# Kernel optimization log

Measured on AMD Instinct MI355X. Metric: run time of the kernel, lower is better.

Reference implementation:

```python
import jax, jax.numpy as jnp
import numpy as np
import math

E = 256          # embed_dim
H = 16           # num_heads
D = E // H       # qkv_dim = 16; also ms_hidden_dim per head
B, R, C = 4, 512, 512


def setup_inputs() -> dict:
    key = jax.random.key(0)
    ks = jax.random.split(key, 9)
    x1 = jax.random.normal(ks[0], (B, R, E), dtype=jnp.float32)
    x2 = jax.random.normal(ks[1], (B, C, E), dtype=jnp.float32)
    cost_mat = jax.random.uniform(ks[2], (B, R, C), dtype=jnp.float32)
    attn_mask = jnp.ones((B, R, C), dtype=bool)
    s = 0.02
    Wqv1 = jax.random.normal(ks[3], (2 * E, E), dtype=jnp.float32) * s   # nn.Linear(E, 2E)
    W1ms = jax.random.normal(ks[4], (H * D, 2 * H), dtype=jnp.float32) * s  # lin1: 2H -> H*D
    W2ms = jax.random.normal(ks[5], (H, H * D), dtype=jnp.float32) * s      # lin2: H*D -> H
    Wo1 = jax.random.normal(ks[6], (E, E), dtype=jnp.float32) * s
    Wo2 = jax.random.normal(ks[7], (E, E), dtype=jnp.float32) * s
    return {"x1": x1, "x2": x2, "cost_mat": cost_mat, "attn_mask": attn_mask,
            "Wqv1": Wqv1, "W1ms": W1ms, "W2ms": W2ms, "Wo1": Wo1, "Wo2": Wo2}


def _apply_weights_and_combine(dots, v):
    # dots: [b h r c], v: [b h c d]
    logits = dots / jnp.std(dots, ddof=1)           # torch .std() is unbiased
    weights = jax.nn.softmax(logits, axis=-1)
    weights = jnp.where(jnp.isnan(weights), 0.0, weights)  # nan_to_num(0)
    out = jnp.einsum('bhrc,bhcd->bhrd', weights, v)
    b, h, s, d = out.shape
    return out.transpose(0, 2, 1, 3).reshape(b, s, h * d)  # 'b h s d -> b s (h d)'


def reference(x1, x2, cost_mat, attn_mask, Wqv1, W1ms, W2ms, Wo1, Wo2):
    b, r, e = x1.shape
    c = x2.shape[1]
    norm = 1.0 / math.sqrt(D)
    # NOTE: source applies Wqv1 to BOTH x1 and x2 (Wkv2 is unused) - kept faithful.
    qv1 = (x1 @ Wqv1.T).reshape(b, r, 2, H, D)
    q = qv1[:, :, 0].transpose(0, 2, 1, 3)   # b h r d
    v1 = qv1[:, :, 1].transpose(0, 2, 1, 3)
    kv2 = (x2 @ Wqv1.T).reshape(b, c, 2, H, D)
    k = kv2[:, :, 0].transpose(0, 2, 1, 3)   # b h c d
    v2 = kv2[:, :, 1].transpose(0, 2, 1, 3)

    dot = norm * jnp.einsum('bhrd,bhcd->bhrc', q, k)       # b h r c
    cost = jnp.broadcast_to(cost_mat[:, None], dot.shape)   # b h r c
    # MixedScoreFF: stack -> 'b h r c s -> b r c (h s)' -> lin1 -> relu -> lin2
    two = jnp.stack([dot, cost], axis=-1)                    # b h r c 2
    two = two.transpose(0, 2, 3, 1, 4).reshape(b, r, c, 2 * H)
    ms1 = jax.nn.relu(two @ W1ms.T)                          # b r c (H*D)
    ms2 = ms1 @ W2ms.T                                       # b r c H
    dot = ms2.transpose(0, 3, 1, 2)                          # b h r c

    mask = jnp.broadcast_to(attn_mask[:, None], dot.shape)
    dot = jnp.where(mask, dot, -jnp.inf)

    h1 = _apply_weights_and_combine(dot, v2) @ Wo1.T                      # b r e
    h2 = _apply_weights_and_combine(dot.transpose(0, 1, 3, 2), v1) @ Wo2.T  # b c e
    return h1, h2
```

## Files before the change

### kernel.cpp

```cpp
#include <hip/hip_runtime.h>
#include <hip/hip_bf16.h>
#include <math.h>
#include <float.h>

#define BB 4
#define RR 512
#define CC 512
#define EE 256
#define HH 16
#define DD 16

typedef short bf16x8 __attribute__((ext_vector_type(8)));
typedef float f32x4 __attribute__((ext_vector_type(4)));
typedef unsigned int uint4v __attribute__((ext_vector_type(4)));
typedef unsigned short u16;
typedef unsigned int u32;

__device__ __forceinline__ void split_bf16(float v, u16& hi, u16& lo)
{
    u32 u = __builtin_bit_cast(u32, v);
    hi = (u16)(u >> 16);
    float hf = __builtin_bit_cast(float, u & 0xffff0000u);
    lo = (u16)(__builtin_bit_cast(u32, v - hf) >> 16);
}

__device__ __forceinline__ void split2(float v0, float v1, u32& hi, u32& lo)
{
    u32 u0 = __builtin_bit_cast(u32, v0);
    u32 u1 = __builtin_bit_cast(u32, v1);
    hi = (u0 >> 16) | (u1 & 0xffff0000u);
    float l0 = v0 - __builtin_bit_cast(float, u0 & 0xffff0000u);
    float l1 = v1 - __builtin_bit_cast(float, u1 & 0xffff0000u);
    lo = (__builtin_bit_cast(u32, l0) >> 16) |
         (__builtin_bit_cast(u32, l1) & 0xffff0000u);
}

__device__ __forceinline__ void split2_cvt(float v0, float v1, u32& hi, u32& lo)
{
    u32 h;
    asm("v_cvt_pk_bf16_f32 %0, %1, %2" : "=v"(h) : "v"(v0), "v"(v1));
    float h0 = __builtin_bit_cast(float, h << 16);
    float h1 = __builtin_bit_cast(float, h & 0xffff0000u);
    float r0 = v0 - h0, r1 = v1 - h1;
    u32 lo_;
    asm("v_cvt_pk_bf16_f32 %0, %1, %2" : "=v"(lo_) : "v"(r0), "v"(r1));
    hi = h; lo = lo_;
}

__device__ __forceinline__ bf16x8 mk8(u32 a, u32 b, u32 c, u32 d)
{
    return __builtin_bit_cast(bf16x8, (uint4v){a, b, c, d});
}

__global__ __launch_bounds__(256) void split_multi(
    const float* __restrict__ s0, u16* __restrict__ h0, u16* __restrict__ l0, int n0,
    const float* __restrict__ s1, u16* __restrict__ h1, u16* __restrict__ l1, int n1,
    const float* __restrict__ s2, u16* __restrict__ h2, u16* __restrict__ l2, int n2,
    const float* __restrict__ s3, u16* __restrict__ h3, u16* __restrict__ l3, int n3,
    const float* __restrict__ s4, u16* __restrict__ h4, u16* __restrict__ l4, int n4)
{
    const float* src; u16* dh; u16* dl; int n;
    switch (blockIdx.y) {
        case 0: src = s0; dh = h0; dl = l0; n = n0; break;
        case 1: src = s1; dh = h1; dl = l1; n = n1; break;
        case 2: src = s2; dh = h2; dl = l2; n = n2; break;
        case 3: src = s3; dh = h3; dl = l3; n = n3; break;
        default: src = s4; dh = h4; dl = l4; n = n4; break;
    }
    for (int i = blockIdx.x * 256 + threadIdx.x; i < n; i += gridDim.x * 256) {
        float4 v = reinterpret_cast<const float4*>(src)[i];
        u32 a0, b0, a1, b1;
        split2(v.x, v.y, a0, b0);
        split2(v.z, v.w, a1, b1);
        reinterpret_cast<uint2*>(dh)[i] = make_uint2(a0, a1);
        reinterpret_cast<uint2*>(dl)[i] = make_uint2(b0, b1);
    }
}

__global__ __launch_bounds__(256) void gemm_mfma(
    const u16* __restrict__ Xh0, const u16* __restrict__ Xl0,
    const u16* __restrict__ Wh0, const u16* __restrict__ Wl0,
    float* __restrict__ Y0,
    const u16* __restrict__ Xh1, const u16* __restrict__ Xl1,
    const u16* __restrict__ Wh1, const u16* __restrict__ Wl1,
    float* __restrict__ Y1,
    int M, int N)
{
    const int t = threadIdx.x;
    const int w = t >> 6, l = t & 63, g = l >> 4, q = l & 15;
    const int z = blockIdx.z;
    const u16* __restrict__ Xh = z ? Xh1 : Xh0;
    const u16* __restrict__ Xl = z ? Xl1 : Xl0;
    const u16* __restrict__ Wh = z ? Wh1 : Wh0;
    const u16* __restrict__ Wl = z ? Wl1 : Wl0;
    float* __restrict__ Y = z ? Y1 : Y0;

    const int m0 = blockIdx.x * 64, n0 = blockIdx.y * 64;
    const size_t arow = (size_t)(m0 + w * 16 + q) * 256;

    f32x4 acc[4] = {};
    #pragma unroll 2
    for (int k0 = 0; k0 < 256; k0 += 32) {
        const bf16x8 ah = *reinterpret_cast<const bf16x8*>(Xh + arow + k0 + g * 8);
        const bf16x8 al = *reinterpret_cast<const bf16x8*>(Xl + arow + k0 + g * 8);
        #pragma unroll
        for (int nt = 0; nt < 4; ++nt) {
            const size_t brow = (size_t)(n0 + nt * 16 + q) * 256;
            const bf16x8 bh = *reinterpret_cast<const bf16x8*>(Wh + brow + k0 + g * 8);
            const bf16x8 bl = *reinterpret_cast<const bf16x8*>(Wl + brow + k0 + g * 8);
            acc[nt] = __builtin_amdgcn_mfma_f32_16x16x32_bf16(ah, bl, acc[nt], 0, 0, 0);
            acc[nt] = __builtin_amdgcn_mfma_f32_16x16x32_bf16(al, bh, acc[nt], 0, 0, 0);
            acc[nt] = __builtin_amdgcn_mfma_f32_16x16x32_bf16(ah, bh, acc[nt], 0, 0, 0);
        }
    }
    #pragma unroll
    for (int nt = 0; nt < 4; ++nt)
        #pragma unroll
        for (int rg = 0; rg < 4; ++rg)
            Y[(size_t)(m0 + w * 16 + g * 4 + rg) * N + n0 + nt * 16 + q] = acc[nt][rg];
}

__global__ void pack_weights(const float* __restrict__ W1,
                             const float* __restrict__ W2,
                             u16* __restrict__ Wb1h, u16* __restrict__ Wb1l,
                             u16* __restrict__ Wb2h, u16* __restrict__ Wb2l)
{
    const int t = threadIdx.x;
    for (int idx = t; idx < 16 * 64 * 8; idx += 256) {
        int nt = idx >> 9, rem = idx & 511, l = rem >> 3, i = rem & 7;
        int k = ((l >> 4) << 3) + i, j = nt * 16 + (l & 15);
        float v = 0.f;
        if (k < 16) {
            v = 0.25f * W1[j * 32 + 2 * k];
        } else if (k == 16) {
            float s = 0.f;
            #pragma unroll
            for (int h = 0; h < 16; ++h) s += W1[j * 32 + 2 * h + 1];
            v = s;
        }
        u16 hi, lo; split_bf16(v, hi, lo);
        Wb1h[idx] = hi; Wb1l[idx] = lo;
    }
    for (int idx = t; idx < 8 * 64 * 8; idx += 256) {
        int kt = idx >> 9, rem = idx & 511, l = rem >> 3, i = rem & 7;
        int jj = kt * 32 + ((l >> 4) << 3) + i, h = l & 15;
        float v = W2[h * 256 + jj];
        u16 hi, lo; split_bf16(v, hi, lo);
        Wb2h[idx] = hi; Wb2l[idx] = lo;
    }
}

__global__ __launch_bounds__(256, 4) void score_ff(
    const float* __restrict__ qv1, const float* __restrict__ kv2,
    const float* __restrict__ cost,
    const u16* __restrict__ Wb1h, const u16* __restrict__ Wb1l,
    const u16* __restrict__ Wb2h, const u16* __restrict__ Wb2l,
    float* __restrict__ S, float* __restrict__ stats)
{
    __shared__ __align__(16) u16 Fhi[16][16][16];
    __shared__ __align__(16) u16 Flo[16][16][16];
    __shared__ __align__(16) float Hs[4][16][32];
    __shared__ float costS[16][16];
    __shared__ __align__(16) f32x4 red[2][4][64];

    const int t = threadIdx.x;
    const int w = t >> 6, l = t & 63;
    const int g = l >> 4, q = l & 15;
    const int b = blockIdx.z;
    const int r0 = blockIdx.y * 16, c0 = blockIdx.x * 16;

    {
        int rr = t >> 4, cc = t & 15;
        costS[rr][cc] = cost[((size_t)b * RR + r0 + rr) * CC + c0 + cc];
    }

    #pragma unroll
    for (int hh = 0; hh < 4; ++hh) {
        const int h = w * 4 + hh;
        bf16x8 qhi = {}, qlo = {}, khi = {}, klo = {};
        if (g < 2) {
            const float4* qp = reinterpret_cast<const float4*>(
                qv1 + ((size_t)b * RR + r0 + q) * (2 * EE) + h * 16 + g * 8);
            const float4* kp = reinterpret_cast<const float4*>(
                kv2 + ((size_t)b * CC + c0 + q) * (2 * EE) + h * 16 + g * 8);
            float4 q0 = qp[0], q1 = qp[1];
            float4 k0 = kp[0], k1 = kp[1];
            u32 a0, a1, a2, a3, b0, b1, b2, b3;
            split2(q0.x, q0.y, a0, b0); split2(q0.z, q0.w, a1, b1);
            split2(q1.x, q1.y, a2, b2); split2(q1.z, q1.w, a3, b3);
            qhi = mk8(a0, a1, a2, a3); qlo = mk8(b0, b1, b2, b3);
            split2(k0.x, k0.y, a0, b0); split2(k0.z, k0.w, a1, b1);
            split2(k1.x, k1.y, a2, b2); split2(k1.z, k1.w, a3, b3);
            khi = mk8(a0, a1, a2, a3); klo = mk8(b0, b1, b2, b3);
        }
        f32x4 d = {0.f, 0.f, 0.f, 0.f};
        d = __builtin_amdgcn_mfma_f32_16x16x32_bf16(qhi, klo, d, 0, 0, 0);
        d = __builtin_amdgcn_mfma_f32_16x16x32_bf16(qlo, khi, d, 0, 0, 0);
        d = __builtin_amdgcn_mfma_f32_16x16x32_bf16(qhi, khi, d, 0, 0, 0);
        #pragma unroll
        for (int rg = 0; rg < 4; ++rg) {
            int r = g * 4 + rg;
            u16 hi, lo; split_bf16(d[rg], hi, lo);
            u32 ad = ((u32)(r * 512 + q * 32 + h * 2)) ^
                     (((((u32)r & 7u) ^ ((u32)q >> 2)) & 7u) << 4);
            *(u16*)((char*)Fhi + ad) = hi;
            *(u16*)((char*)Flo + ad) = lo;
        }
    }

    bf16x8 w1h_r[4], w1l_r[4], w2h_r[2], w2l_r[2];
    #pragma unroll
    for (int jt = 0; jt < 4; ++jt) {
        int nt = w * 4 + jt;
        w1h_r[jt] = *reinterpret_cast<const bf16x8*>(Wb1h + ((nt * 64 + l) << 3));
        w1l_r[jt] = *reinterpret_cast<const bf16x8*>(Wb1l + ((nt * 64 + l) << 3));
    }
    #pragma unroll
    for (int kk = 0; kk < 2; ++kk) {
        int kt = w * 2 + kk;
        w2h_r[kk] = *reinterpret_cast<const bf16x8*>(Wb2h + ((kt * 64 + l) << 3));
        w2l_r[kk] = *reinterpret_cast<const bf16x8*>(Wb2l + ((kt * 64 + l) << 3));
    }
    __syncthreads();

    float lsum = 0.f, lsq = 0.f;
    char* hw = (char*)&Hs[w][0][0];
    const u32 hswz = ((u32)q & 7u) << 4;

    for (int rr = 0; rr < 16; ++rr) {
        bf16x8 fhi = {}, flo = {};
        {
            const u32 fswz = (((((u32)rr & 7u) ^ ((u32)q >> 2)) & 7u) << 4);
            if (g < 2) {
                u32 fa = ((u32)(rr * 512 + q * 32 + g * 16)) ^ fswz;
                fhi = *reinterpret_cast<const bf16x8*>((char*)Fhi + fa);
                flo = *reinterpret_cast<const bf16x8*>((char*)Flo + fa);
            } else if (g == 2) {
                u16 chi, clo; split_bf16(costS[rr][q], chi, clo);
                fhi[0] = (short)chi; flo[0] = (short)clo;
            }
        }

        f32x4 acc2 = {0.f, 0.f, 0.f, 0.f};
        #pragma unroll
        for (int ch = 0; ch < 2; ++ch) {
            #pragma unroll
            for (int jt2 = 0; jt2 < 2; ++jt2) {
                int jt = ch * 2 + jt2;
                f32x4 a = {0.f, 0.f, 0.f, 0.f};
                a = __builtin_amdgcn_mfma_f32_16x16x32_bf16(w1h_r[jt], flo, a, 0, 0, 0);
                a = __builtin_amdgcn_mfma_f32_16x16x32_bf16(w1l_r[jt], fhi, a, 0, 0, 0);
                a = __builtin_amdgcn_mfma_f32_16x16x32_bf16(w1h_r[jt], fhi, a, 0, 0, 0);
                f32x4 hrel;
                #pragma unroll
                for (int rg = 0; rg < 4; ++rg) hrel[rg] = fmaxf(a[rg], 0.f);
                u32 ad = ((u32)(q * 128 + jt2 * 64 + g * 16)) ^ hswz;
                *reinterpret_cast<f32x4*>(hw + ad) = hrel;
            }
            const f32x4 h0 = *reinterpret_cast<const f32x4*>(
                hw + (((u32)(q * 128 + g * 32)) ^ hswz));
            const f32x4 h1 = *reinterpret_cast<const f32x4*>(
                hw + (((u32)(q * 128 + g * 32 + 16)) ^ hswz));
            u32 hh0, hl0, hh1, hl1, hh2, hl2, hh3, hl3;
            split2_cvt(h0[0], h0[1], hh0, hl0); split2_cvt(h0[2], h0[3], hh1, hl1);
            split2_cvt(h1[0], h1[1], hh2, hl2); split2_cvt(h1[2], h1[3], hh3, hl3);
            const bf16x8 ha = mk8(hh0, hh1, hh2, hh3);
            const bf16x8 hb = mk8(hl0, hl1, hl2, hl3);
            acc2 = __builtin_amdgcn_mfma_f32_16x16x32_bf16(ha, w2l_r[ch], acc2, 0, 0, 0);
            acc2 = __builtin_amdgcn_mfma_f32_16x16x32_bf16(hb, w2h_r[ch], acc2, 0, 0, 0);
            acc2 = __builtin_amdgcn_mfma_f32_16x16x32_bf16(ha, w2h_r[ch], acc2, 0, 0, 0);
        }

        if (rr > 0) {
            int pr = rr - 1, par = pr & 1;
            f32x4 s4 = red[par][0][l] + red[par][1][l] + red[par][2][l] + red[par][3][l];
            float v = (w & 2) ? ((w & 1) ? s4[3] : s4[2])
                              : ((w & 1) ? s4[1] : s4[0]);
            lsum += v; lsq = fmaf(v, v, lsq);
            S[(((size_t)b * HH + q) * RR + r0 + pr) * CC + c0 + g * 4 + w] = v;
        }

        red[rr & 1][w][l] = acc2;
        __syncthreads();
    }
    {
        f32x4 s4 = red[1][0][l] + red[1][1][l] + red[1][2][l] + red[1][3][l];
        float v = (w & 2) ? ((w & 1) ? s4[3] : s4[2])
                          : ((w & 1) ? s4[1] : s4[0]);
        lsum += v; lsq = fmaf(v, v, lsq);
        S[(((size_t)b * HH + q) * RR + r0 + 15) * CC + c0 + g * 4 + w] = v;
    }

    #pragma unroll
    for (int s = 32; s; s >>= 1) {
        lsum += __shfl_xor(lsum, s);
        lsq  += __shfl_xor(lsq, s);
    }
    if (l == 0) {
        int bucket = (((blockIdx.x + blockIdx.y * 8 + blockIdx.z * 32) << 2) + w) & 127;
        atomicAdd(&stats[2 * bucket],     lsum);
        atomicAdd(&stats[2 * bucket + 1], lsq);
    }
}

__global__ void finalize_std(const float* __restrict__ stats,
                             float* __restrict__ invstd)
{
    double sum = 0.0, sq = 0.0;
    for (int i = 0; i < 128; ++i) { sum += (double)stats[2 * i]; sq += (double)stats[2 * i + 1]; }
    double N = (double)BB * HH * RR * CC;
    double mean = sum / N;
    double var = (sq - N * mean * mean) / (N - 1.0);
    float inv = (var > 0.0 && isfinite(var)) ? (float)(1.0 / sqrt(var)) : nanf("");
    *invstd = inv;
}

__global__ __launch_bounds__(256, 4) void attn_rows(
    const float* __restrict__ S, const float* __restrict__ kv2,
    const float* __restrict__ invstd_p,
    u16* __restrict__ a1h, u16* __restrict__ a1l)
{
    __shared__ __align__(16) u16 Vthi[16 * 512];
    __shared__ __align__(16) u16 Vtlo[16 * 512];

    const int t = threadIdx.x;
    const int w = t >> 6, l = t & 63;
    const int g = l >> 4, q = l & 15;
    const int b = blockIdx.z, h = blockIdx.y;
    const int r0 = blockIdx.x * 64 + w * 16;
    const float inv = *invstd_p;

    {
        const float* v0p = kv2 + ((size_t)b * CC + 2 * t) * (2 * EE) + EE + h * DD;
        const float* v1p = v0p + 2 * EE;
        float4 va[4], vb[4];
        #pragma unroll
        for (int j = 0; j < 4; ++j) {
            va[j] = reinterpret_cast<const float4*>(v0p)[j];
            vb[j] = reinterpret_cast<const float4*>(v1p)[j];
        }
        const float* vaf = reinterpret_cast<const float*>(va);
        const float* vbf = reinterpret_cast<const float*>(vb);
        #pragma unroll
        for (int d = 0; d < 16; ++d) {
            u32 hi, lo; split2(vaf[d], vbf[d], hi, lo);
            u32 ad = ((u32)d * 1024 + (u32)t * 4) ^ (((u32)d & 7) << 4);
            *reinterpret_cast<u32*>((char*)Vthi + ad) = hi;
            *reinterpret_cast<u32*>((char*)Vtlo + ad) = lo;
        }
    }
    __syncthreads();

    float lsum = 0.f;
    f32x4 acc = {0.f, 0.f, 0.f, 0.f};
    #pragma unroll 4
    for (int kt = 0; kt < 16; ++kt) {
        const float* sp = S + (((size_t)b * HH + h) * RR + r0 + q) * CC + kt * 32 + g * 8;
        float4 s0 = reinterpret_cast<const float4*>(sp)[0];
        float4 s1 = reinterpret_cast<const float4*>(sp)[1];
        float p[8];
        p[0] = __expf(s0.x * inv); p[1] = __expf(s0.y * inv);
        p[2] = __expf(s0.z * inv); p[3] = __expf(s0.w * inv);
        p[4] = __expf(s1.x * inv); p[5] = __expf(s1.y * inv);
        p[6] = __expf(s1.z * inv); p[7] = __expf(s1.w * inv);
        lsum += (p[0] + p[1]) + (p[2] + p[3]) + (p[4] + p[5]) + (p[6] + p[7]);
        u32 ph[4], pl[4];
        split2(p[0], p[1], ph[0], pl[0]); split2(p[2], p[3], ph[1], pl[1]);
        split2(p[4], p[5], ph[2], pl[2]); split2(p[6], p[7], ph[3], pl[3]);
        const bf16x8 phi = mk8(ph[0], ph[1], ph[2], ph[3]);
        const bf16x8 plo = mk8(pl[0], pl[1], pl[2], pl[3]);
        u32 A = ((u32)q * 1024 + (u32)(kt * 64 + g * 16)) ^ (((u32)q & 7) << 4);
        const bf16x8 vhi = *reinterpret_cast<const bf16x8*>((char*)Vthi + A);
        const bf16x8 vlo = *reinterpret_cast<const bf16x8*>((char*)Vtlo + A);
        acc = __builtin_amdgcn_mfma_f32_16x16x32_bf16(phi, vlo, acc, 0, 0, 0);
        acc = __builtin_amdgcn_mfma_f32_16x16x32_bf16(plo, vhi, acc, 0, 0, 0);
        acc = __builtin_amdgcn_mfma_f32_16x16x32_bf16(phi, vhi, acc, 0, 0, 0);
    }
    lsum += __shfl_xor(lsum, 16);
    lsum += __shfl_xor(lsum, 32);

    #pragma unroll
    for (int rg = 0; rg < 4; ++rg) {
        int row = g * 4 + rg;
        float L = __shfl(lsum, row);
        bool valid = (L > 0.f) && isfinite(L);
        float rl = valid ? 1.f / L : 0.f;
        float v = acc[rg] * rl;
        u16 hi, lo; split_bf16(v, hi, lo);
        size_t off = ((size_t)b * RR + r0 + row) * EE + h * DD + q;
        a1h[off] = hi; a1l[off] = lo;
    }
}

__global__ __launch_bounds__(256, 4) void attn_cols(
    const float* __restrict__ S, const float* __restrict__ qv1,
    const float* __restrict__ invstd_p,
    u16* __restrict__ a2h, u16* __restrict__ a2l)
{
    __shared__ __align__(16) u16 Vthi[16 * 512];
    __shared__ __align__(16) u16 Vtlo[16 * 512];

    const int t = threadIdx.x;
    const int w = t >> 6, l = t & 63;
    const int g = l >> 4, q = l & 15;
    const int b = blockIdx.z, h = blockIdx.y;
    const int c0 = blockIdx.x * 64 + w * 16;
    const float inv = *invstd_p;

    {
        const float* v0p = qv1 + ((size_t)b * RR + 2 * t) * (2 * EE) + EE + h * DD;
        const float* v1p = v0p + 2 * EE;
        float4 va[4], vb[4];
        #pragma unroll
        for (int j = 0; j < 4; ++j) {
            va[j] = reinterpret_cast<const float4*>(v0p)[j];
            vb[j] = reinterpret_cast<const float4*>(v1p)[j];
        }
        const float* vaf = reinterpret_cast<const float*>(va);
        const float* vbf = reinterpret_cast<const float*>(vb);
        #pragma unroll
        for (int d = 0; d < 16; ++d) {
            u32 hi, lo; split2(vaf[d], vbf[d], hi, lo);
            u32 ad = ((u32)d * 1024 + (u32)t * 4) ^ (((u32)d & 7) << 4);
            *reinterpret_cast<u32*>((char*)Vthi + ad) = hi;
            *reinterpret_cast<u32*>((char*)Vtlo + ad) = lo;
        }
    }
    __syncthreads();

    float lsum = 0.f;
    f32x4 acc = {0.f, 0.f, 0.f, 0.f};
    #pragma unroll 4
    for (int kt = 0; kt < 16; ++kt) {
        const float* sp = S + (((size_t)b * HH + h) * RR + kt * 32 + g * 8) * CC + c0 + q;
        float p[8];
        #pragma unroll
        for (int i = 0; i < 8; ++i)
            p[i] = __expf(sp[(size_t)i * CC] * inv);
        lsum += (p[0] + p[1]) + (p[2] + p[3]) + (p[4] + p[5]) + (p[6] + p[7]);
        u32 ph[4], pl[4];
        split2(p[0], p[1], ph[0], pl[0]); split2(p[2], p[3], ph[1], pl[1]);
        split2(p[4], p[5], ph[2], pl[2]); split2(p[6], p[7], ph[3], pl[3]);
        const bf16x8 phi = mk8(ph[0], ph[1], ph[2], ph[3]);
        const bf16x8 plo = mk8(pl[0], pl[1], pl[2], pl[3]);
        u32 A = ((u32)q * 1024 + (u32)(kt * 64 + g * 16)) ^ (((u32)q & 7) << 4);
        const bf16x8 vhi = *reinterpret_cast<const bf16x8*>((char*)Vthi + A);
        const bf16x8 vlo = *reinterpret_cast<const bf16x8*>((char*)Vtlo + A);
        acc = __builtin_amdgcn_mfma_f32_16x16x32_bf16(phi, vlo, acc, 0, 0, 0);
        acc = __builtin_amdgcn_mfma_f32_16x16x32_bf16(plo, vhi, acc, 0, 0, 0);
        acc = __builtin_amdgcn_mfma_f32_16x16x32_bf16(phi, vhi, acc, 0, 0, 0);
    }
    lsum += __shfl_xor(lsum, 16);
    lsum += __shfl_xor(lsum, 32);

    #pragma unroll
    for (int rg = 0; rg < 4; ++rg) {
        int row = g * 4 + rg;
        float L = __shfl(lsum, row);
        bool valid = (L > 0.f) && isfinite(L);
        float rl = valid ? 1.f / L : 0.f;
        float v = acc[rg] * rl;
        u16 hi, lo; split_bf16(v, hi, lo);
        size_t off = ((size_t)b * CC + c0 + row) * EE + h * DD + q;
        a2h[off] = hi; a2l[off] = lo;
    }
}

extern "C" void kernel_launch(void* const* d_in, const int* in_sizes, int n_in,
                              void* d_out, int out_size, void* d_ws, size_t ws_size,
                              hipStream_t stream)
{
    const float* x1   = (const float*)d_in[0];
    const float* x2   = (const float*)d_in[1];
    const float* cost = (const float*)d_in[2];
    const float* Wqv1 = (const float*)d_in[4];
    const float* W1ms = (const float*)d_in[5];
    const float* W2ms = (const float*)d_in[6];
    const float* Wo1  = (const float*)d_in[7];
    const float* Wo2  = (const float*)d_in[8];

    float* ws    = (float*)d_ws;
    float* qv1   = ws;
    float* kv2   = qv1 + (size_t)1048576;
    float* S     = kv2 + (size_t)1048576;
    float* A1    = S + (size_t)16777216;
    float* A2    = A1 + (size_t)524288;
    float* stats = A2 + (size_t)524288;
    float* invstd = stats + 256;
    u16* Wb1h = (u16*)(invstd + 4);
    u16* Wb1l = Wb1h + 8192;
    u16* Wb2h = Wb1l + 8192;
    u16* Wb2l = Wb2h + 4096;
    u16* x1h  = Wb2l + 4096;
    u16* x1l  = x1h + 524288;
    u16* x2h  = x1l + 524288;
    u16* x2l  = x2h + 524288;
    u16* wqh  = x2l + 524288;
    u16* wql  = wqh + 131072;
    u16* wo1h = wql + 131072;
    u16* wo1l = wo1h + 65536;
    u16* wo2h = wo1l + 65536;
    u16* wo2l = wo2h + 65536;
    u16* a1h  = wo2l + 65536;
    u16* a1l  = a1h + 524288;
    u16* a2h  = a1l + 524288;
    u16* a2l  = a2h + 524288;

    hipMemsetAsync(stats, 0, 256 * sizeof(float), stream);

    pack_weights<<<1, 256, 0, stream>>>(W1ms, W2ms, Wb1h, Wb1l, Wb2h, Wb2l);
    split_multi<<<dim3(128, 5), 256, 0, stream>>>(
        x1, x1h, x1l, 131072,
        x2, x2h, x2l, 131072,
        Wqv1, wqh, wql, 32768,
        Wo1, wo1h, wo1l, 16384,
        Wo2, wo2h, wo2l, 16384);

    gemm_mfma<<<dim3(32, 8, 2), 256, 0, stream>>>(
        x1h, x1l, wqh, wql, qv1,
        x2h, x2l, wqh, wql, kv2, 2048, 512);

    score_ff<<<dim3(32, 32, 4), 256, 0, stream>>>(qv1, kv2, cost,
                                                  Wb1h, Wb1l, Wb2h, Wb2l, S, stats);
    finalize_std<<<1, 1, 0, stream>>>(stats, invstd);
    attn_rows<<<dim3(8, 16, 4), 256, 0, stream>>>(S, kv2, invstd, a1h, a1l);
    attn_cols<<<dim3(8, 16, 4), 256, 0, stream>>>(S, qv1, invstd, a2h, a2l);

    gemm_mfma<<<dim3(32, 4, 2), 256, 0, stream>>>(
        a1h, a1l, wo1h, wo1l, (float*)d_out,
        a2h, a2l, wo2h, wo2l, (float*)d_out + (size_t)2048 * 256, 2048, 256);
}
```

Baseline: 198.1 us.

## Fuse attention row/col kernels, inline std finalize, merge weight packing launch

Merges attn_rows and attn_cols into one launch with a doubled grid. The single-thread finalize_std kernel is replaced by a per-wave shuffle reduction of the stats in every attention block. pack_weights becomes an extra blockIdx.y slice of split_multi. score_ff drops its double-buffered reduction in favour of a single buffer with two barriers per row, and its occupancy hint rises to 5 blocks. The aim is fewer launches and less serialization, at the cost of extra syncs in score_ff and of computing the variance in float instead of double.

```diff
diff --git a/kernel.cpp b/kernel.cpp
--- a/kernel.cpp
+++ b/kernel.cpp
@@ -52,13 +52,60 @@
     return __builtin_bit_cast(bf16x8, (uint4v){a, b, c, d});
 }
 
+__device__ __forceinline__ float compute_invstd(const float* __restrict__ stats,
+                                                int l)
+{
+    float se = stats[2 * l] + stats[2 * l + 128];
+    float sq = stats[2 * l + 1] + stats[2 * l + 129];
+    #pragma unroll
+    for (int s = 32; s; s >>= 1) {
+        se += __shfl_xor(se, s);
+        sq += __shfl_xor(sq, s);
+    }
+    const float Nf = 16777216.f;
+    float mean = se / Nf;
+    float var = (sq - Nf * mean * mean) / (Nf - 1.f);
+    bool ok = (var > 0.f) && isfinite(var);
+    return ok ? (1.f / sqrtf(var)) : __builtin_nanf("");
+}
+
 __global__ __launch_bounds__(256) void split_multi(
     const float* __restrict__ s0, u16* __restrict__ h0, u16* __restrict__ l0, int n0,
     const float* __restrict__ s1, u16* __restrict__ h1, u16* __restrict__ l1, int n1,
     const float* __restrict__ s2, u16* __restrict__ h2, u16* __restrict__ l2, int n2,
     const float* __restrict__ s3, u16* __restrict__ h3, u16* __restrict__ l3, int n3,
-    const float* __restrict__ s4, u16* __restrict__ h4, u16* __restrict__ l4, int n4)
-{
+    const float* __restrict__ s4, u16* __restrict__ h4, u16* __restrict__ l4, int n4,
+    const float* __restrict__ W1, const float* __restrict__ W2,
+    u16* __restrict__ Wb1h, u16* __restrict__ Wb1l,
+    u16* __restrict__ Wb2h, u16* __restrict__ Wb2l)
+{
+    const int t = threadIdx.x;
+    if (blockIdx.y == 5) {
+        if (blockIdx.x != 0) return;
+        for (int idx = t; idx < 16 * 64 * 8; idx += 256) {
+            int nt = idx >> 9, rem = idx & 511, l = rem >> 3, i = rem & 7;
+            int k = ((l >> 4) << 3) + i, j = nt * 16 + (l & 15);
+            float v = 0.f;
+            if (k < 16) {
+                v = 0.25f * W1[j * 32 + 2 * k];
+            } else if (k == 16) {
+                float s = 0.f;
+                #pragma unroll
+                for (int h = 0; h < 16; ++h) s += W1[j * 32 + 2 * h + 1];
+                v = s;
+            }
+            u16 hi, lo; split_bf16(v, hi, lo);
+            Wb1h[idx] = hi; Wb1l[idx] = lo;
+        }
+        for (int idx = t; idx < 8 * 64 * 8; idx += 256) {
+            int kt = idx >> 9, rem = idx & 511, l = rem >> 3, i = rem & 7;
+            int jj = kt * 32 + ((l >> 4) << 3) + i, h = l & 15;
+            float v = W2[h * 256 + jj];
+            u16 hi, lo; split_bf16(v, hi, lo);
+            Wb2h[idx] = hi; Wb2l[idx] = lo;
+        }
+        return;
+    }
     const float* src; u16* dh; u16* dl; int n;
     switch (blockIdx.y) {
         case 0: src = s0; dh = h0; dl = l0; n = n0; break;
@@ -67,7 +114,7 @@
         case 3: src = s3; dh = h3; dl = l3; n = n3; break;
         default: src = s4; dh = h4; dl = l4; n = n4; break;
     }
-    for (int i = blockIdx.x * 256 + threadIdx.x; i < n; i += gridDim.x * 256) {
+    for (int i = blockIdx.x * 256 + t; i < n; i += gridDim.x * 256) {
         float4 v = reinterpret_cast<const float4*>(src)[i];
         u32 a0, b0, a1, b1;
         split2(v.x, v.y, a0, b0);
@@ -120,37 +167,7 @@
             Y[(size_t)(m0 + w * 16 + g * 4 + rg) * N + n0 + nt * 16 + q] = acc[nt][rg];
 }
 
-__global__ void pack_weights(const float* __restrict__ W1,
-                             const float* __restrict__ W2,
-                             u16* __restrict__ Wb1h, u16* __restrict__ Wb1l,
-                             u16* __restrict__ Wb2h, u16* __restrict__ Wb2l)
-{
-    const int t = threadIdx.x;
-    for (int idx = t; idx < 16 * 64 * 8; idx += 256) {
-        int nt = idx >> 9, rem = idx & 511, l = rem >> 3, i = rem & 7;
-        int k = ((l >> 4) << 3) + i, j = nt * 16 + (l & 15);
-        float v = 0.f;
-        if (k < 16) {
-            v = 0.25f * W1[j * 32 + 2 * k];
-        } else if (k == 16) {
-            float s = 0.f;
-            #pragma unroll
-            for (int h = 0; h < 16; ++h) s += W1[j * 32 + 2 * h + 1];
-            v = s;
-        }
-        u16 hi, lo; split_bf16(v, hi, lo);
-        Wb1h[idx] = hi; Wb1l[idx] = lo;
-    }
-    for (int idx = t; idx < 8 * 64 * 8; idx += 256) {
-        int kt = idx >> 9, rem = idx & 511, l = rem >> 3, i = rem & 7;
-        int jj = kt * 32 + ((l >> 4) << 3) + i, h = l & 15;
-        float v = W2[h * 256 + jj];
-        u16 hi, lo; split_bf16(v, hi, lo);
-        Wb2h[idx] = hi; Wb2l[idx] = lo;
-    }
-}
-
-__global__ __launch_bounds__(256, 4) void score_ff(
+__global__ __launch_bounds__(256, 5) void score_ff(
     const float* __restrict__ qv1, const float* __restrict__ kv2,
     const float* __restrict__ cost,
     const u16* __restrict__ Wb1h, const u16* __restrict__ Wb1l,
@@ -161,7 +178,7 @@
     __shared__ __align__(16) u16 Flo[16][16][16];
     __shared__ __align__(16) float Hs[4][16][32];
     __shared__ float costS[16][16];
-    __shared__ __align__(16) f32x4 red[2][4][64];
+    __shared__ __align__(16) f32x4 red[4][64];
 
     const int t = threadIdx.x;
     const int w = t >> 6, l = t & 63;
@@ -271,24 +288,16 @@
             acc2 = __builtin_amdgcn_mfma_f32_16x16x32_bf16(ha, w2h_r[ch], acc2, 0, 0, 0);
         }
 
-        if (rr > 0) {
-            int pr = rr - 1, par = pr & 1;
-            f32x4 s4 = red[par][0][l] + red[par][1][l] + red[par][2][l] + red[par][3][l];
+        red[w][l] = acc2;
+        __syncthreads();
+        {
+            f32x4 s4 = red[0][l] + red[1][l] + red[2][l] + red[3][l];
             float v = (w & 2) ? ((w & 1) ? s4[3] : s4[2])
                               : ((w & 1) ? s4[1] : s4[0]);
             lsum += v; lsq = fmaf(v, v, lsq);
-            S[(((size_t)b * HH + q) * RR + r0 + pr) * CC + c0 + g * 4 + w] = v;
-        }
-
-        red[rr & 1][w][l] = acc2;
+            S[(((size_t)b * HH + q) * RR + r0 + rr) * CC + c0 + g * 4 + w] = v;
+        }
         __syncthreads();
-    }
-    {
-        f32x4 s4 = red[1][0][l] + red[1][1][l] + red[1][2][l] + red[1][3][l];
-        float v = (w & 2) ? ((w & 1) ? s4[3] : s4[2])
-                          : ((w & 1) ? s4[1] : s4[0]);
-        lsum += v; lsq = fmaf(v, v, lsq);
-        S[(((size_t)b * HH + q) * RR + r0 + 15) * CC + c0 + g * 4 + w] = v;
     }
 
     #pragma unroll
@@ -303,22 +312,11 @@
     }
 }
 
-__global__ void finalize_std(const float* __restrict__ stats,
-                             float* __restrict__ invstd)
-{
-    double sum = 0.0, sq = 0.0;
-    for (int i = 0; i < 128; ++i) { sum += (double)stats[2 * i]; sq += (double)stats[2 * i + 1]; }
-    double N = (double)BB * HH * RR * CC;
-    double mean = sum / N;
-    double var = (sq - N * mean * mean) / (N - 1.0);
-    float inv = (var > 0.0 && isfinite(var)) ? (float)(1.0 / sqrt(var)) : nanf("");
-    *invstd = inv;
-}
-
-__global__ __launch_bounds__(256, 4) void attn_rows(
+__global__ __launch_bounds__(256, 4) void attn_fused(
     const float* __restrict__ S, const float* __restrict__ kv2,
-    const float* __restrict__ invstd_p,
-    u16* __restrict__ a1h, u16* __restrict__ a1l)
+    const float* __restrict__ qv1, const float* __restrict__ stats,
+    u16* __restrict__ a1h, u16* __restrict__ a1l,
+    u16* __restrict__ a2h, u16* __restrict__ a2l)
 {
     __shared__ __align__(16) u16 Vthi[16 * 512];
     __shared__ __align__(16) u16 Vtlo[16 * 512];
@@ -326,12 +324,14 @@
     const int t = threadIdx.x;
     const int w = t >> 6, l = t & 63;
     const int g = l >> 4, q = l & 15;
-    const int b = blockIdx.z, h = blockIdx.y;
-    const int r0 = blockIdx.x * 64 + w * 16;
-    const float inv = *invstd_p;
+    const bool rows = (blockIdx.z < 4);
+    const int b = rows ? blockIdx.z : (blockIdx.z - 4);
+    const int h = blockIdx.y;
+    const float inv = compute_invstd(stats, l);
 
     {
-        const float* v0p = kv2 + ((size_t)b * CC + 2 * t) * (2 * EE) + EE + h * DD;
+        const float* vbase = rows ? kv2 : qv1;
+        const float* v0p = vbase + ((size_t)b * 512 + 2 * t) * (2 * EE) + EE + h * DD;
         const float* v1p = v0p + 2 * EE;
         float4 va[4], vb[4];
         #pragma unroll
@@ -351,34 +351,62 @@
     }
     __syncthreads();
 
+    const int x0 = blockIdx.x * 64 + w * 16;
     float lsum = 0.f;
     f32x4 acc = {0.f, 0.f, 0.f, 0.f};
-    #pragma unroll 4
-    for (int kt = 0; kt < 16; ++kt) {
-        const float* sp = S + (((size_t)b * HH + h) * RR + r0 + q) * CC + kt * 32 + g * 8;
-        float4 s0 = reinterpret_cast<const float4*>(sp)[0];
-        float4 s1 = reinterpret_cast<const float4*>(sp)[1];
-        float p[8];
-        p[0] = __expf(s0.x * inv); p[1] = __expf(s0.y * inv);
-        p[2] = __expf(s0.z * inv); p[3] = __expf(s0.w * inv);
-        p[4] = __expf(s1.x * inv); p[5] = __expf(s1.y * inv);
-        p[6] = __expf(s1.z * inv); p[7] = __expf(s1.w * inv);
-        lsum += (p[0] + p[1]) + (p[2] + p[3]) + (p[4] + p[5]) + (p[6] + p[7]);
-        u32 ph[4], pl[4];
-        split2(p[0], p[1], ph[0], pl[0]); split2(p[2], p[3], ph[1], pl[1]);
-        split2(p[4], p[5], ph[2], pl[2]); split2(p[6], p[7], ph[3], pl[3]);
-        const bf16x8 phi = mk8(ph[0], ph[1], ph[2], ph[3]);
-        const bf16x8 plo = mk8(pl[0], pl[1], pl[2], pl[3]);
-        u32 A = ((u32)q * 1024 + (u32)(kt * 64 + g * 16)) ^ (((u32)q & 7) << 4);
-        const bf16x8 vhi = *reinterpret_cast<const bf16x8*>((char*)Vthi + A);
-        const bf16x8 vlo = *reinterpret_cast<const bf16x8*>((char*)Vtlo + A);
-        acc = __builtin_amdgcn_mfma_f32_16x16x32_bf16(phi, vlo, acc, 0, 0, 0);
-        acc = __builtin_amdgcn_mfma_f32_16x16x32_bf16(plo, vhi, acc, 0, 0, 0);
-        acc = __builtin_amdgcn_mfma_f32_16x16x32_bf16(phi, vhi, acc, 0, 0, 0);
-    }
+
+    if (rows) {
+        #pragma unroll 4
+        for (int kt = 0; kt < 16; ++kt) {
+            const float* sp = S + (((size_t)b * HH + h) * RR + x0 + q) * CC + kt * 32 + g * 8;
+            float4 s0 = reinterpret_cast<const float4*>(sp)[0];
+            float4 s1 = reinterpret_cast<const float4*>(sp)[1];
+            float p[8];
+            p[0] = __expf(s0.x * inv); p[1] = __expf(s0.y * inv);
+            p[2] = __expf(s0.z * inv); p[3] = __expf(s0.w * inv);
+            p[4] = __expf(s1.x * inv); p[5] = __expf(s1.y * inv);
+            p[6] = __expf(s1.z * inv); p[7] = __expf(s1.w * inv);
+            lsum += (p[0] + p[1]) + (p[2] + p[3]) + (p[4] + p[5]) + (p[6] + p[7]);
+            u32 ph[4], pl[4];
+            split2(p[0], p[1], ph[0], pl[0]); split2(p[2], p[3], ph[1], pl[1]);
+            split2(p[4], p[5], ph[2], pl[2]); split2(p[6], p[7], ph[3], pl[3]);
+            const bf16x8 phi = mk8(ph[0], ph[1], ph[2], ph[3]);
+            const bf16x8 plo = mk8(pl[0], pl[1], pl[2], pl[3]);
+            u32 A = ((u32)q * 1024 + (u32)(kt * 64 + g * 16)) ^ (((u32)q & 7) << 4);
+            const bf16x8 vhi = *reinterpret_cast<const bf16x8*>((char*)Vthi + A);
+            const bf16x8 vlo = *reinterpret_cast<const bf16x8*>((char*)Vtlo + A);
+            acc = __builtin_amdgcn_mfma_f32_16x16x32_bf16(phi, vlo, acc, 0, 0, 0);
+            acc = __builtin_amdgcn_mfma_f32_16x16x32_bf16(plo, vhi, acc, 0, 0, 0);
+            acc = __builtin_amdgcn_mfma_f32_16x16x32_bf16(phi, vhi, acc, 0, 0, 0);
+        }
+    } else {
+        #pragma unroll 4
+        for (int kt = 0; kt < 16; ++kt) {
+            const float* sp = S + (((size_t)b * HH + h) * RR + kt * 32 + g * 8) * CC + x0 + q;
+            float p[8];
+            #pragma unroll
+            for (int i = 0; i < 8; ++i)
+                p[i] = __expf(sp[(size_t)i * CC] * inv);
+            lsum += (p[0] + p[1]) + (p[2] + p[3]) + (p[4] + p[5]) + (p[6] + p[7]);
+            u32 ph[4], pl[4];
+            split2(p[0], p[1], ph[0], pl[0]); split2(p[2], p[3], ph[1], pl[1]);
+            split2(p[4], p[5], ph[2], pl[2]); split2(p[6], p[7], ph[3], pl[3]);
+            const bf16x8 phi = mk8(ph[0], ph[1], ph[2], ph[3]);
+            const bf16x8 plo = mk8(pl[0], pl[1], pl[2], pl[3]);
+            u32 A = ((u32)q * 1024 + (u32)(kt * 64 + g * 16)) ^ (((u32)q & 7) << 4);
+            const bf16x8 vhi = *reinterpret_cast<const bf16x8*>((char*)Vthi + A);
+            const bf16x8 vlo = *reinterpret_cast<const bf16x8*>((char*)Vtlo + A);
+            acc = __builtin_amdgcn_mfma_f32_16x16x32_bf16(phi, vlo, acc, 0, 0, 0);
+            acc = __builtin_amdgcn_mfma_f32_16x16x32_bf16(plo, vhi, acc, 0, 0, 0);
+            acc = __builtin_amdgcn_mfma_f32_16x16x32_bf16(phi, vhi, acc, 0, 0, 0);
+        }
+    }
+
     lsum += __shfl_xor(lsum, 16);
     lsum += __shfl_xor(lsum, 32);
 
+    u16* dh = rows ? a1h : a2h;
+    u16* dl = rows ? a1l : a2l;
     #pragma unroll
     for (int rg = 0; rg < 4; ++rg) {
         int row = g * 4 + rg;
@@ -387,82 +415,8 @@
         float rl = valid ? 1.f / L : 0.f;
         float v = acc[rg] * rl;
         u16 hi, lo; split_bf16(v, hi, lo);
-        size_t off = ((size_t)b * RR + r0 + row) * EE + h * DD + q;
-        a1h[off] = hi; a1l[off] = lo;
-    }
-}
-
-__global__ __launch_bounds__(256, 4) void attn_cols(
-    const float* __restrict__ S, const float* __restrict__ qv1,
-    const float* __restrict__ invstd_p,
-    u16* __restrict__ a2h, u16* __restrict__ a2l)
-{
-    __shared__ __align__(16) u16 Vthi[16 * 512];
-    __shared__ __align__(16) u16 Vtlo[16 * 512];
-
-    const int t = threadIdx.x;
-    const int w = t >> 6, l = t & 63;
-    const int g = l >> 4, q = l & 15;
-    const int b = blockIdx.z, h = blockIdx.y;
-    const int c0 = blockIdx.x * 64 + w * 16;
-    const float inv = *invstd_p;
-
-    {
-        const float* v0p = qv1 + ((size_t)b * RR + 2 * t) * (2 * EE) + EE + h * DD;
-        const float* v1p = v0p + 2 * EE;
-        float4 va[4], vb[4];
-        #pragma unroll
-        for (int j = 0; j < 4; ++j) {
-            va[j] = reinterpret_cast<const float4*>(v0p)[j];
-            vb[j] = reinterpret_cast<const float4*>(v1p)[j];
-        }
-        const float* vaf = reinterpret_cast<const float*>(va);
-        const float* vbf = reinterpret_cast<const float*>(vb);
-        #pragma unroll
-        for (int d = 0; d < 16; ++d) {
-            u32 hi, lo; split2(vaf[d], vbf[d], hi, lo);
-            u32 ad = ((u32)d * 1024 + (u32)t * 4) ^ (((u32)d & 7) << 4);
-            *reinterpret_cast<u32*>((char*)Vthi + ad) = hi;
-            *reinterpret_cast<u32*>((char*)Vtlo + ad) = lo;
-        }
-    }
-    __syncthreads();
-
-    float lsum = 0.f;
-    f32x4 acc = {0.f, 0.f, 0.f, 0.f};
-    #pragma unroll 4
-    for (int kt = 0; kt < 16; ++kt) {
-        const float* sp = S + (((size_t)b * HH + h) * RR + kt * 32 + g * 8) * CC + c0 + q;
-        float p[8];
-        #pragma unroll
-        for (int i = 0; i < 8; ++i)
-            p[i] = __expf(sp[(size_t)i * CC] * inv);
-        lsum += (p[0] + p[1]) + (p[2] + p[3]) + (p[4] + p[5]) + (p[6] + p[7]);
-        u32 ph[4], pl[4];
-        split2(p[0], p[1], ph[0], pl[0]); split2(p[2], p[3], ph[1], pl[1]);
-        split2(p[4], p[5], ph[2], pl[2]); split2(p[6], p[7], ph[3], pl[3]);
-        const bf16x8 phi = mk8(ph[0], ph[1], ph[2], ph[3]);
-        const bf16x8 plo = mk8(pl[0], pl[1], pl[2], pl[3]);
-        u32 A = ((u32)q * 1024 + (u32)(kt * 64 + g * 16)) ^ (((u32)q & 7) << 4);
-        const bf16x8 vhi = *reinterpret_cast<const bf16x8*>((char*)Vthi + A);
-        const bf16x8 vlo = *reinterpret_cast<const bf16x8*>((char*)Vtlo + A);
-        acc = __builtin_amdgcn_mfma_f32_16x16x32_bf16(phi, vlo, acc, 0, 0, 0);
-        acc = __builtin_amdgcn_mfma_f32_16x16x32_bf16(plo, vhi, acc, 0, 0, 0);
-        acc = __builtin_amdgcn_mfma_f32_16x16x32_bf16(phi, vhi, acc, 0, 0, 0);
-    }
-    lsum += __shfl_xor(lsum, 16);
-    lsum += __shfl_xor(lsum, 32);
-
-    #pragma unroll
-    for (int rg = 0; rg < 4; ++rg) {
-        int row = g * 4 + rg;
-        float L = __shfl(lsum, row);
-        bool valid = (L > 0.f) && isfinite(L);
-        float rl = valid ? 1.f / L : 0.f;
-        float v = acc[rg] * rl;
-        u16 hi, lo; split_bf16(v, hi, lo);
-        size_t off = ((size_t)b * CC + c0 + row) * EE + h * DD + q;
-        a2h[off] = hi; a2l[off] = lo;
+        size_t off = ((size_t)b * 512 + x0 + row) * EE + h * DD + q;
+        dh[off] = hi; dl[off] = lo;
     }
 }
 
@@ -483,9 +437,7 @@
     float* qv1   = ws;
     float* kv2   = qv1 + (size_t)1048576;
     float* S     = kv2 + (size_t)1048576;
-    float* A1    = S + (size_t)16777216;
-    float* A2    = A1 + (size_t)524288;
-    float* stats = A2 + (size_t)524288;
+    float* stats = S + (size_t)16777216;
     float* invstd = stats + 256;
     u16* Wb1h = (u16*)(invstd + 4);
     u16* Wb1l = Wb1h + 8192;
@@ -508,13 +460,13 @@
 
     hipMemsetAsync(stats, 0, 256 * sizeof(float), stream);
 
-    pack_weights<<<1, 256, 0, stream>>>(W1ms, W2ms, Wb1h, Wb1l, Wb2h, Wb2l);
-    split_multi<<<dim3(128, 5), 256, 0, stream>>>(
+    split_multi<<<dim3(128, 6), 256, 0, stream>>>(
         x1, x1h, x1l, 131072,
         x2, x2h, x2l, 131072,
         Wqv1, wqh, wql, 32768,
         Wo1, wo1h, wo1l, 16384,
-        Wo2, wo2h, wo2l, 16384);
+        Wo2, wo2h, wo2l, 16384,
+        W1ms, W2ms, Wb1h, Wb1l, Wb2h, Wb2l);
 
     gemm_mfma<<<dim3(32, 8, 2), 256, 0, stream>>>(
         x1h, x1l, wqh, wql, qv1,
@@ -522,9 +474,9 @@
 
     score_ff<<<dim3(32, 32, 4), 256, 0, stream>>>(qv1, kv2, cost,
                                                   Wb1h, Wb1l, Wb2h, Wb2l, S, stats);
-    finalize_std<<<1, 1, 0, stream>>>(stats, invstd);
-    attn_rows<<<dim3(8, 16, 4), 256, 0, stream>>>(S, kv2, invstd, a1h, a1l);
-    attn_cols<<<dim3(8, 16, 4), 256, 0, stream>>>(S, qv1, invstd, a2h, a2l);
+
+    attn_fused<<<dim3(8, 16, 8), 256, 0, stream>>>(S, kv2, qv1, stats,
+                                                   a1h, a1l, a2h, a2l);
 
     gemm_mfma<<<dim3(32, 4, 2), 256, 0, stream>>>(
         a1h, a1l, wo1h, wo1l, (float*)d_out,
```

After: 200.6 us. No clear change (+1.3%).
